# Optimization experiments

Measured on AMD Instinct MI355X. Metric: run time of the kernel, lower is better.

## Reference

```python
import jax, jax.numpy as jnp
import numpy as np

N_NODES = 100000
N_EDGES = 1600000
IN_F = 32
HID_F = 128  # unused by the torch module's GCN (only conv1), kept for fidelity
OUT_F = 64


def setup_inputs() -> dict:
    key = jax.random.key(0)
    ks = jax.random.split(key, 8)
    x = jax.random.normal(ks[0], (N_NODES, IN_F), dtype=jnp.float32)
    edge_index = jax.random.randint(ks[1], (2, N_EDGES), 0, N_NODES, dtype=jnp.int64)
    s = 1.0 / np.sqrt(IN_F)
    # SAGEConv params: lin_l acts on mean-aggregated neighbors (with bias), lin_r on root
    W_l = jax.random.uniform(ks[2], (IN_F, OUT_F), minval=-s, maxval=s, dtype=jnp.float32)
    W_r = jax.random.uniform(ks[3], (IN_F, OUT_F), minval=-s, maxval=s, dtype=jnp.float32)
    b_l = jnp.zeros((OUT_F,), dtype=jnp.float32)
    # MLPPredictor: lin1 (2*OUT_F -> OUT_F), lin2 (OUT_F -> 1)
    s1 = 1.0 / np.sqrt(2 * OUT_F)
    W1 = jax.random.uniform(ks[4], (2 * OUT_F, OUT_F), minval=-s1, maxval=s1, dtype=jnp.float32)
    b1 = jnp.zeros((OUT_F,), dtype=jnp.float32)
    s2 = 1.0 / np.sqrt(OUT_F)
    W2 = jax.random.uniform(ks[5], (OUT_F, 1), minval=-s2, maxval=s2, dtype=jnp.float32)
    b2 = jnp.zeros((1,), dtype=jnp.float32)
    return {"x": x, "edge_index": edge_index, "W_l": W_l, "W_r": W_r, "b_l": b_l,
            "W1": W1, "b1": b1, "W2": W2, "b2": b2}


def reference(x, edge_index, W_l, W_r, b_l, W1, b1, W2, b2):
    src = edge_index[0]  # sender / message source
    dst = edge_index[1]  # receiver / aggregation target
    n = x.shape[0]
    # SAGEConv with mean aggregation: out_i = lin_l(mean_{j->i} x_j) + lin_r(x_i)
    agg = jax.ops.segment_sum(x[src], dst, num_segments=n)  # [N, IN_F]
    cnt = jax.ops.segment_sum(jnp.ones((src.shape[0],), x.dtype), dst, num_segments=n)
    mean_agg = agg / jnp.maximum(cnt, 1.0)[:, None]
    h = jnp.tanh(mean_agg @ W_l + b_l + x @ W_r)  # [N, OUT_F]
    # MLPPredictor: per-edge concat(sender, receiver) -> lin1 -> tanh -> lin2 -> tanh
    he = jnp.concatenate([h[src], h[dst]], axis=-1)  # [E, 2*OUT_F]
    he = jnp.tanh(he @ W1 + b1)
    he = jnp.tanh(he @ W2 + b2)  # [E, 1]
    return jax.nn.sigmoid(he)
```

## Files before the change

kernel.cpp:

```cpp
#include <hip/hip_runtime.h>
#include <hip/hip_bf16.h>

#define NN 100000
#define NE 1600000
#define INF 32
#define OUTF 64

typedef __hip_bfloat16 bf16;
typedef unsigned long long u64;
typedef __attribute__((ext_vector_type(8))) short short8v;
typedef __attribute__((ext_vector_type(4))) float float4v;
typedef __attribute__((ext_vector_type(2))) float floatx2;

__device__ __forceinline__ float load_f(const void* p, long long i, int f32) {
  return f32 ? ((const float*)p)[i] : __bfloat162float(((const bf16*)p)[i]);
}
__device__ __forceinline__ int load_idx(const void* p, long long i, int i64) {
  return i64 ? (int)((const long long*)p)[i] : ((const int*)p)[i];
}
__device__ __forceinline__ float fast_tanh(float x) {
  float e = __expf(2.0f * x);
  return 1.0f - 2.0f * __builtin_amdgcn_rcpf(e + 1.0f);
}
__device__ __forceinline__ bf16 f2b(float f) { return __float2bfloat16(f); }
__device__ __forceinline__ short bf_bits(float f) {
  bf16 h = __float2bfloat16(f);
  return *reinterpret_cast<short*>(&h);
}
__device__ __forceinline__ unsigned enc_fx(float v) {
  v = fminf(fmaxf(v, -7.99f), 7.99f);
  return (unsigned)rintf((v + 8.0f) * 64.0f);
}
__device__ __forceinline__ unsigned char f2fp8(float f) {
  unsigned p = __builtin_amdgcn_cvt_pk_fp8_f32(f, f, 0, false);
  return (unsigned char)(p & 0xFF);
}

__global__ void k_detect(const void* __restrict__ x, const void* __restrict__ ei,
                         int* __restrict__ flags)
{
  int t = threadIdx.x;
  const unsigned* xu = (const unsigned*)x;
  int hits = 0;
  #pragma unroll
  for (int i = 0; i < 16; ++i) {
    unsigned w = xu[t * 16 + i];
    unsigned mid = (w >> 7) & 0xFF;
    hits += (mid >= 0x70 && mid <= 0x86) ? 1 : 0;
  }
  #pragma unroll
  for (int off = 32; off > 0; off >>= 1) hits += __shfl_xor(hits, off, 64);
  const int* e32 = (const int*)ei;
  unsigned long long m = __ballot(e32[2 * t + 1] == 0);
  if (t == 0) {
    flags[0] = (hits < 512) ? 1 : 0;
    flags[1] = (m == ~0ULL) ? 1 : 0;
  }
}

__global__ __launch_bounds__(256)
void k_prep(const void* __restrict__ x, u64* __restrict__ penc,
            const int* __restrict__ flags)
{
  int xf32 = flags[0];
  int i = blockIdx.x * 256 + threadIdx.x;
  float v0, v1, v2, v3;
  if (xf32) {
    float4 v = ((const float4*)x)[i];
    v0 = v.x; v1 = v.y; v2 = v.z; v3 = v.w;
  } else {
    uint2 w = ((const uint2*)x)[i];
    v0 = __uint_as_float(w.x << 16);
    v1 = __uint_as_float(w.x & 0xffff0000u);
    v2 = __uint_as_float(w.y << 16);
    v3 = __uint_as_float(w.y & 0xffff0000u);
  }
  penc[i] = (u64)enc_fx(v0) | ((u64)enc_fx(v1) << 16)
          | ((u64)enc_fx(v2) << 32) | ((u64)enc_fx(v3) << 48);
}

__global__ __launch_bounds__(256)
void k_agg(const u64* __restrict__ penc, const void* __restrict__ ei,
           u64* __restrict__ pa, int* __restrict__ icnt,
           const int* __restrict__ flags)
{
  int ei64 = flags[1];
  long long gid = (long long)blockIdx.x * 256 + threadIdx.x;
  int e = (int)(gid >> 3);
  int lane = threadIdx.x & 63;
  int q = lane & 7;
  int iv = 0;
  if (q < 2) iv = load_idx(ei, (q ? (long long)NE : 0) + e, ei64);
  int base = lane & ~7;
  int src = __shfl(iv, base, 64);
  int dst = __shfl(iv, base | 1, 64);
  u64 pk = penc[(long long)src * 8 + q];
  atomicAdd(&pa[(long long)dst * 8 + q], pk);
  if (q == 0) atomicAdd(&icnt[dst], 1);
}

__global__ __launch_bounds__(256)
void k_node_uv(const void* __restrict__ x, const u64* __restrict__ pa,
               const int* __restrict__ icnt,
               const void* __restrict__ Wl, const void* __restrict__ Wr,
               const void* __restrict__ bl,
               const void* __restrict__ W1, const void* __restrict__ b1,
               unsigned char* __restrict__ U8, unsigned char* __restrict__ V8,
               const int* __restrict__ flags)
{
  __shared__ bf16 sh[4][16][64];
  __shared__ __align__(16) unsigned char sU[4][16][64];
  __shared__ __align__(16) unsigned char sV[4][16][64];
  int xf32 = flags[0];
  int lane = threadIdx.x & 63, wv = threadIdx.x >> 6;
  int r = lane & 15, g = lane >> 4;

  short8v Bh[2][4];
  #pragma unroll
  for (int kb = 0; kb < 2; ++kb) {
    const void* W = kb ? Wr : Wl;
    #pragma unroll
    for (int nb = 0; nb < 4; ++nb) {
      short8v v;
      #pragma unroll
      for (int e = 0; e < 8; ++e)
        v[e] = bf_bits(load_f(W, (long long)(8 * g + e) * 64 + nb * 16 + r, xf32));
      Bh[kb][nb] = v;
    }
  }
  short8v Bf[4][4];
  #pragma unroll
  for (int kb = 0; kb < 4; ++kb)
    #pragma unroll
    for (int nb = 0; nb < 4; ++nb) {
      short8v v;
      #pragma unroll
      for (int e = 0; e < 8; ++e)
        v[e] = bf_bits(load_f(W1, (long long)(kb * 32 + 8 * g + e) * 64 + nb * 16 + r, xf32));
      Bf[kb][nb] = v;
    }
  float blv[4], b1v[4];
  #pragma unroll
  for (int nb = 0; nb < 4; ++nb) {
    blv[nb] = load_f(bl, nb * 16 + r, xf32);
    b1v[nb] = load_f(b1, nb * 16 + r, xf32);
  }

  const int NT2 = NN / 16;
  int nw = gridDim.x * 4;
  for (int t = blockIdx.x * 4 + wv; t < NT2; t += nw) {
    int n0 = t * 16;
    int node = n0 + r;
    int cnt = icnt[node];
    float s = (cnt > 0) ? __builtin_amdgcn_rcpf(64.0f * cnt) : 0.0f;
    float bias = (cnt > 0) ? 8.0f : 0.0f;
    u64 p0 = pa[(long long)node * 8 + 2 * g];
    u64 p1 = pa[(long long)node * 8 + 2 * g + 1];
    short8v A0, A1;
    #pragma unroll
    for (int j = 0; j < 4; ++j) {
      A0[j]     = bf_bits((float)((p0 >> (16 * j)) & 0xffff) * s - bias);
      A0[4 + j] = bf_bits((float)((p1 >> (16 * j)) & 0xffff) * s - bias);
    }
    if (xf32) {
      const float* xp = (const float*)x + (long long)node * 32 + 8 * g;
      #pragma unroll
      for (int e = 0; e < 8; ++e) A1[e] = bf_bits(xp[e]);
    } else {
      A1 = *(const short8v*)((const bf16*)x + (long long)node * 32 + 8 * g);
    }

    #pragma unroll
    for (int nb = 0; nb < 4; ++nb) {
      float4v acc = (float4v){blv[nb], blv[nb], blv[nb], blv[nb]};
      acc = __builtin_amdgcn_mfma_f32_16x16x32_bf16(A0, Bh[0][nb], acc, 0, 0, 0);
      acc = __builtin_amdgcn_mfma_f32_16x16x32_bf16(A1, Bh[1][nb], acc, 0, 0, 0);
      #pragma unroll
      for (int j = 0; j < 4; ++j)
        sh[wv][4 * g + j][nb * 16 + r] = f2b(fast_tanh(acc[j]));
    }
    asm volatile("s_waitcnt lgkmcnt(0)" ::: "memory");
    __builtin_amdgcn_sched_barrier(0);
    short8v Ah0 = *(const short8v*)&sh[wv][r][8 * g];
    short8v Ah1 = *(const short8v*)&sh[wv][r][32 + 8 * g];

    #pragma unroll
    for (int nb = 0; nb < 4; ++nb) {
      float4v au = (float4v){b1v[nb], b1v[nb], b1v[nb], b1v[nb]};
      au = __builtin_amdgcn_mfma_f32_16x16x32_bf16(Ah0, Bf[0][nb], au, 0, 0, 0);
      au = __builtin_amdgcn_mfma_f32_16x16x32_bf16(Ah1, Bf[1][nb], au, 0, 0, 0);
      float4v av = (float4v){0.0f, 0.0f, 0.0f, 0.0f};
      av = __builtin_amdgcn_mfma_f32_16x16x32_bf16(Ah0, Bf[2][nb], av, 0, 0, 0);
      av = __builtin_amdgcn_mfma_f32_16x16x32_bf16(Ah1, Bf[3][nb], av, 0, 0, 0);
      #pragma unroll
      for (int j = 0; j < 4; ++j) {
        sU[wv][4 * g + j][nb * 16 + r] = f2fp8(au[j]);
        sV[wv][4 * g + j][nb * 16 + r] = f2fp8(av[j]);
      }
    }
    asm volatile("s_waitcnt lgkmcnt(0)" ::: "memory");
    __builtin_amdgcn_sched_barrier(0);

    uint4 stu = *(const uint4*)&sU[wv][r][g * 16];
    uint4 stv = *(const uint4*)&sV[wv][r][g * 16];
    *(uint4*)(U8 + (long long)(n0 + r) * 64 + g * 16) = stu;
    *(uint4*)(V8 + (long long)(n0 + r) * 64 + g * 16) = stv;
    asm volatile("s_waitcnt lgkmcnt(0)" ::: "memory");
    __builtin_amdgcn_sched_barrier(0);
  }
}

struct UV8 { uint4 u, v; };

__device__ __forceinline__ int ld_idx16(const void* ei, long long t, int NT,
                                        int lane, int ei64)
{
  long long tt = (t < NT) ? t : (NT - 1);
  long long e0 = tt * 16;
  int iv = 0;
  if (lane < 32) {
    long long off = (lane < 16) ? (e0 + lane) : ((long long)NE + e0 + (lane - 16));
    iv = ei64 ? (int)((const long long*)ei)[off] : ((const int*)ei)[off];
  }
  return iv;
}
__device__ __forceinline__ UV8 ld_uv8(const unsigned char* U8, const unsigned char* V8,
                                      int iv, int e4, int j)
{
  int sB = __shfl(iv, e4, 64);
  int dB = __shfl(iv, 16 + e4, 64);
  UV8 f;
  f.u = *(const uint4*)(U8 + (long long)sB * 64 + j * 16);
  f.v = *(const uint4*)(V8 + (long long)dB * 64 + j * 16);
  return f;
}

__global__ __launch_bounds__(256)
void k_edge2(const unsigned char* __restrict__ U8, const unsigned char* __restrict__ V8,
             const void* __restrict__ ei,
             const void* __restrict__ W2, const void* __restrict__ b2,
             void* __restrict__ outv, const int* __restrict__ flags)
{
  int xf32 = flags[0], ei64 = flags[1];
  int lane = threadIdx.x & 63, wv = threadIdx.x >> 6;
  int e4 = lane >> 2, j = lane & 3;
  float w2v[16];
  #pragma unroll
  for (int i = 0; i < 16; ++i) w2v[i] = load_f(W2, 16 * j + i, xf32);
  float b2v = load_f(b2, 0, xf32);

  const int NT = NE / 16;
  int nw = gridDim.x * 4;
  long long w0 = blockIdx.x * 4 + wv;

  int i0 = ld_idx16(ei, w0, NT, lane, ei64);
  int i1 = ld_idx16(ei, w0 + nw, NT, lane, ei64);
  int i2 = ld_idx16(ei, w0 + 2 * (long long)nw, NT, lane, ei64);
  UV8 uv0 = ld_uv8(U8, V8, i0, e4, j);
  UV8 uv1 = ld_uv8(U8, V8, i1, e4, j);

  for (long long t = w0; t < NT; t += nw) {
    int i3 = ld_idx16(ei, t + 3 * (long long)nw, NT, lane, ei64);
    UV8 uv2 = ld_uv8(U8, V8, i2, e4, j);

    unsigned ua[4] = {uv0.u.x, uv0.u.y, uv0.u.z, uv0.u.w};
    unsigned va[4] = {uv0.v.x, uv0.v.y, uv0.v.z, uv0.v.w};
    float z = 0.0f;
    #pragma unroll
    for (int d = 0; d < 4; ++d) {
      floatx2 ul = __builtin_amdgcn_cvt_pk_f32_fp8(ua[d], false);
      floatx2 uh = __builtin_amdgcn_cvt_pk_f32_fp8(ua[d], true);
      floatx2 vl = __builtin_amdgcn_cvt_pk_f32_fp8(va[d], false);
      floatx2 vh = __builtin_amdgcn_cvt_pk_f32_fp8(va[d], true);
      z += fast_tanh(ul.x + vl.x) * w2v[4 * d + 0];
      z += fast_tanh(ul.y + vl.y) * w2v[4 * d + 1];
      z += fast_tanh(uh.x + vh.x) * w2v[4 * d + 2];
      z += fast_tanh(uh.y + vh.y) * w2v[4 * d + 3];
    }
    z += __shfl_xor(z, 1, 64);
    z += __shfl_xor(z, 2, 64);
    if (j == 0) {
      float y = fast_tanh(z + b2v);
      float res = __builtin_amdgcn_rcpf(1.0f + __expf(-y));
      long long eo = t * 16 + e4;
      if (xf32) ((float*)outv)[eo] = res;
      else      ((bf16*)outv)[eo] = f2b(res);
    }
    i2 = i3;
    uv0 = uv1;
    uv1 = uv2;
  }
}

extern "C" void kernel_launch(void* const* d_in, const int* in_sizes, int n_in,
                              void* d_out, int out_size, void* d_ws, size_t ws_size,
                              hipStream_t stream)
{
  const void* x  = d_in[0];
  const void* ei = d_in[1];
  const void* Wl = d_in[2];
  const void* Wr = d_in[3];
  const void* bl = d_in[4];
  const void* W1 = d_in[5];
  const void* b1 = d_in[6];
  const void* W2 = d_in[7];
  const void* b2 = d_in[8];

  char* ws = (char*)d_ws;
  u64*  pa    = (u64*)ws;
  int*  icnt  = (int*)(ws + 6400000);
  int*  flags = (int*)(ws + 6800000);
  u64*  penc  = (u64*)(ws + 6800128);
  unsigned char* U8 = (unsigned char*)(ws + 13200128);
  unsigned char* V8 = (unsigned char*)(ws + 19600128);

  k_detect<<<1, 64, 0, stream>>>(x, ei, flags);
  hipMemsetAsync(pa, 0, 6800000, stream);

  k_prep<<<(NN * 8) / 256, 256, 0, stream>>>(x, penc, flags);
  k_agg<<<(NE * 8) / 256, 256, 0, stream>>>(penc, ei, pa, icnt, flags);
  k_node_uv<<<512, 256, 0, stream>>>(x, pa, icnt, Wl, Wr, bl, W1, b1, U8, V8, flags);
  k_edge2<<<2048, 256, 0, stream>>>(U8, V8, ei, W2, b2, d_out, flags);
}
```

Baseline: 319.1 us.

## Replace atomic fixed-point scatter aggregation with CSR sort and segmented mean

The per-edge 64-bit atomic scatter of fixed-point encoded features is replaced by a counting sort of edges by destination (histogram, three-pass scan, atomic scatter of source ids), followed by a gather-based segmented mean that writes bf16 means directly. The node kernel now reads the precomputed bf16 mean instead of decoding fixed-point sums, and its grid grows. The aim is to remove the heavy contention of 8 atomics per edge on the aggregation buffer, at the cost of several extra launches and an atomic scatter pass. Workspace buffers are reused between stages (U8/V8 alias xb and sorted).

```diff
diff --git a/kernel.cpp b/kernel.cpp
--- a/kernel.cpp
+++ b/kernel.cpp
@@ -23,13 +23,12 @@
   return 1.0f - 2.0f * __builtin_amdgcn_rcpf(e + 1.0f);
 }
 __device__ __forceinline__ bf16 f2b(float f) { return __float2bfloat16(f); }
-__device__ __forceinline__ short bf_bits(float f) {
+__device__ __forceinline__ unsigned short bf_bits(float f) {
   bf16 h = __float2bfloat16(f);
-  return *reinterpret_cast<short*>(&h);
-}
-__device__ __forceinline__ unsigned enc_fx(float v) {
-  v = fminf(fmaxf(v, -7.99f), 7.99f);
-  return (unsigned)rintf((v + 8.0f) * 64.0f);
+  return *reinterpret_cast<unsigned short*>(&h);
+}
+__device__ __forceinline__ float s2f(unsigned short s) {
+  return __uint_as_float(((unsigned)s) << 16);
 }
 __device__ __forceinline__ unsigned char f2fp8(float f) {
   unsigned p = __builtin_amdgcn_cvt_pk_fp8_f32(f, f, 0, false);
@@ -59,49 +58,122 @@
 }
 
 __global__ __launch_bounds__(256)
-void k_prep(const void* __restrict__ x, u64* __restrict__ penc,
-            const int* __restrict__ flags)
+void k_xb(const void* __restrict__ x, u64* __restrict__ xb,
+          const int* __restrict__ flags)
 {
   int xf32 = flags[0];
   int i = blockIdx.x * 256 + threadIdx.x;
-  float v0, v1, v2, v3;
   if (xf32) {
     float4 v = ((const float4*)x)[i];
-    v0 = v.x; v1 = v.y; v2 = v.z; v3 = v.w;
+    xb[i] = (u64)bf_bits(v.x) | ((u64)bf_bits(v.y) << 16)
+          | ((u64)bf_bits(v.z) << 32) | ((u64)bf_bits(v.w) << 48);
   } else {
-    uint2 w = ((const uint2*)x)[i];
-    v0 = __uint_as_float(w.x << 16);
-    v1 = __uint_as_float(w.x & 0xffff0000u);
-    v2 = __uint_as_float(w.y << 16);
-    v3 = __uint_as_float(w.y & 0xffff0000u);
-  }
-  penc[i] = (u64)enc_fx(v0) | ((u64)enc_fx(v1) << 16)
-          | ((u64)enc_fx(v2) << 32) | ((u64)enc_fx(v3) << 48);
-}
-
-__global__ __launch_bounds__(256)
-void k_agg(const u64* __restrict__ penc, const void* __restrict__ ei,
-           u64* __restrict__ pa, int* __restrict__ icnt,
-           const int* __restrict__ flags)
+    xb[i] = ((const u64*)x)[i];
+  }
+}
+
+__global__ __launch_bounds__(256)
+void k_hist(const void* __restrict__ ei, int* __restrict__ cnt,
+            const int* __restrict__ flags)
 {
   int ei64 = flags[1];
-  long long gid = (long long)blockIdx.x * 256 + threadIdx.x;
-  int e = (int)(gid >> 3);
-  int lane = threadIdx.x & 63;
-  int q = lane & 7;
-  int iv = 0;
-  if (q < 2) iv = load_idx(ei, (q ? (long long)NE : 0) + e, ei64);
-  int base = lane & ~7;
-  int src = __shfl(iv, base, 64);
-  int dst = __shfl(iv, base | 1, 64);
-  u64 pk = penc[(long long)src * 8 + q];
-  atomicAdd(&pa[(long long)dst * 8 + q], pk);
-  if (q == 0) atomicAdd(&icnt[dst], 1);
-}
-
-__global__ __launch_bounds__(256)
-void k_node_uv(const void* __restrict__ x, const u64* __restrict__ pa,
-               const int* __restrict__ icnt,
+  int e = blockIdx.x * 256 + threadIdx.x;
+  int dst = load_idx(ei, (long long)NE + e, ei64);
+  atomicAdd(&cnt[dst], 1);
+}
+
+__global__ __launch_bounds__(256)
+void k_scan1(const int* __restrict__ cnt, int* __restrict__ off,
+             int* __restrict__ sums)
+{
+  __shared__ int s[256];
+  int t = threadIdx.x;
+  int i = blockIdx.x * 256 + t;
+  int v = (i < NN) ? cnt[i] : 0;
+  s[t] = v;
+  __syncthreads();
+  #pragma unroll
+  for (int d = 1; d < 256; d <<= 1) {
+    int y = (t >= d) ? s[t - d] : 0;
+    __syncthreads();
+    s[t] += y;
+    __syncthreads();
+  }
+  if (i < NN) off[i] = s[t] - v;
+  if (t == 255) sums[blockIdx.x] = s[255];
+}
+
+__global__ __launch_bounds__(512)
+void k_scan2(int* __restrict__ sums)
+{
+  __shared__ int s[512];
+  int t = threadIdx.x;
+  int v = (t < 391) ? sums[t] : 0;
+  s[t] = v;
+  __syncthreads();
+  #pragma unroll
+  for (int d = 1; d < 512; d <<= 1) {
+    int y = (t >= d) ? s[t - d] : 0;
+    __syncthreads();
+    s[t] += y;
+    __syncthreads();
+  }
+  if (t < 391) sums[t] = s[t] - v;
+}
+
+__global__ __launch_bounds__(256)
+void k_scan3(int* __restrict__ off, int* __restrict__ off2,
+             const int* __restrict__ sums)
+{
+  int i = blockIdx.x * 256 + threadIdx.x;
+  if (i < NN) {
+    int o = off[i] + sums[blockIdx.x];
+    off[i] = o;
+    off2[i] = o;
+  }
+}
+
+__global__ __launch_bounds__(256)
+void k_scatter(const void* __restrict__ ei, int* __restrict__ off2,
+               int* __restrict__ sorted, const int* __restrict__ flags)
+{
+  int ei64 = flags[1];
+  int e = blockIdx.x * 256 + threadIdx.x;
+  int src = load_idx(ei, e, ei64);
+  int dst = load_idx(ei, (long long)NE + e, ei64);
+  int pos = atomicAdd(&off2[dst], 1);
+  sorted[pos] = src;
+}
+
+__global__ __launch_bounds__(256)
+void k_segmean(const u64* __restrict__ xb, const int* __restrict__ sorted,
+               const int* __restrict__ off, const int* __restrict__ cnt,
+               u64* __restrict__ meanb)
+{
+  int lane = threadIdx.x & 63, wv = threadIdx.x >> 6;
+  int grp = lane >> 3, q = lane & 7;
+  int dst = (blockIdx.x * 4 + wv) * 8 + grp;
+  int begin = off[dst];
+  int n = cnt[dst];
+  float a0 = 0.f, a1 = 0.f, a2 = 0.f, a3 = 0.f;
+  int src = (n > 0) ? sorted[begin] : 0;
+  for (int k = 0; k < n; ++k) {
+    int srcN = (k + 1 < n) ? sorted[begin + k + 1] : 0;
+    u64 w = xb[(long long)src * 8 + q];
+    a0 += s2f((unsigned short)(w & 0xffff));
+    a1 += s2f((unsigned short)((w >> 16) & 0xffff));
+    a2 += s2f((unsigned short)((w >> 32) & 0xffff));
+    a3 += s2f((unsigned short)((w >> 48) & 0xffff));
+    src = srcN;
+  }
+  float sc = __builtin_amdgcn_rcpf(fmaxf((float)n, 1.0f));
+  meanb[(long long)dst * 8 + q] =
+      (u64)bf_bits(a0 * sc) | ((u64)bf_bits(a1 * sc) << 16)
+    | ((u64)bf_bits(a2 * sc) << 32) | ((u64)bf_bits(a3 * sc) << 48);
+}
+
+__global__ __launch_bounds__(256)
+void k_node_uv(const void* __restrict__ x, const u64* __restrict__ meanb,
                const void* __restrict__ Wl, const void* __restrict__ Wr,
                const void* __restrict__ bl,
                const void* __restrict__ W1, const void* __restrict__ b1,
@@ -124,7 +196,7 @@
       short8v v;
       #pragma unroll
       for (int e = 0; e < 8; ++e)
-        v[e] = bf_bits(load_f(W, (long long)(8 * g + e) * 64 + nb * 16 + r, xf32));
+        v[e] = (short)bf_bits(load_f(W, (long long)(8 * g + e) * 64 + nb * 16 + r, xf32));
       Bh[kb][nb] = v;
     }
   }
@@ -136,7 +208,7 @@
       short8v v;
       #pragma unroll
       for (int e = 0; e < 8; ++e)
-        v[e] = bf_bits(load_f(W1, (long long)(kb * 32 + 8 * g + e) * 64 + nb * 16 + r, xf32));
+        v[e] = (short)bf_bits(load_f(W1, (long long)(kb * 32 + 8 * g + e) * 64 + nb * 16 + r, xf32));
       Bf[kb][nb] = v;
     }
   float blv[4], b1v[4];
@@ -151,21 +223,12 @@
   for (int t = blockIdx.x * 4 + wv; t < NT2; t += nw) {
     int n0 = t * 16;
     int node = n0 + r;
-    int cnt = icnt[node];
-    float s = (cnt > 0) ? __builtin_amdgcn_rcpf(64.0f * cnt) : 0.0f;
-    float bias = (cnt > 0) ? 8.0f : 0.0f;
-    u64 p0 = pa[(long long)node * 8 + 2 * g];
-    u64 p1 = pa[(long long)node * 8 + 2 * g + 1];
-    short8v A0, A1;
-    #pragma unroll
-    for (int j = 0; j < 4; ++j) {
-      A0[j]     = bf_bits((float)((p0 >> (16 * j)) & 0xffff) * s - bias);
-      A0[4 + j] = bf_bits((float)((p1 >> (16 * j)) & 0xffff) * s - bias);
-    }
+    short8v A0 = *(const short8v*)((const char*)meanb + (long long)node * 64 + g * 16);
+    short8v A1;
     if (xf32) {
       const float* xp = (const float*)x + (long long)node * 32 + 8 * g;
       #pragma unroll
-      for (int e = 0; e < 8; ++e) A1[e] = bf_bits(xp[e]);
+      for (int e = 0; e < 8; ++e) A1[e] = (short)bf_bits(xp[e]);
     } else {
       A1 = *(const short8v*)((const bf16*)x + (long long)node * 32 + 8 * g);
     }
@@ -307,18 +370,27 @@
   const void* b2 = d_in[8];
 
   char* ws = (char*)d_ws;
-  u64*  pa    = (u64*)ws;
-  int*  icnt  = (int*)(ws + 6400000);
-  int*  flags = (int*)(ws + 6800000);
-  u64*  penc  = (u64*)(ws + 6800128);
-  unsigned char* U8 = (unsigned char*)(ws + 13200128);
-  unsigned char* V8 = (unsigned char*)(ws + 19600128);
+  int* flags  = (int*)(ws);
+  int* cnt    = (int*)(ws + 1024);
+  int* off    = (int*)(ws + 401408);
+  int* off2   = (int*)(ws + 801792);
+  int* sums   = (int*)(ws + 1202176);
+  int* sorted = (int*)(ws + 1208320);
+  u64* xb     = (u64*)(ws + 7608320);
+  u64* meanb  = (u64*)(ws + 14008320);
+  unsigned char* U8 = (unsigned char*)(ws + 7608320);
+  unsigned char* V8 = (unsigned char*)(ws + 1208320);
 
   k_detect<<<1, 64, 0, stream>>>(x, ei, flags);
-  hipMemsetAsync(pa, 0, 6800000, stream);
-
-  k_prep<<<(NN * 8) / 256, 256, 0, stream>>>(x, penc, flags);
-  k_agg<<<(NE * 8) / 256, 256, 0, stream>>>(penc, ei, pa, icnt, flags);
-  k_node_uv<<<512, 256, 0, stream>>>(x, pa, icnt, Wl, Wr, bl, W1, b1, U8, V8, flags);
+  hipMemsetAsync(cnt, 0, 400000, stream);
+
+  k_xb<<<3125, 256, 0, stream>>>(x, xb, flags);
+  k_hist<<<6250, 256, 0, stream>>>(ei, cnt, flags);
+  k_scan1<<<391, 256, 0, stream>>>(cnt, off, sums);
+  k_scan2<<<1, 512, 0, stream>>>(sums);
+  k_scan3<<<391, 256, 0, stream>>>(off, off2, sums);
+  k_scatter<<<6250, 256, 0, stream>>>(ei, off2, sorted, flags);
+  k_segmean<<<3125, 256, 0, stream>>>(xb, sorted, off, cnt, meanb);
+  k_node_uv<<<1563, 256, 0, stream>>>(x, meanb, Wl, Wr, bl, W1, b1, U8, V8, flags);
   k_edge2<<<2048, 256, 0, stream>>>(U8, V8, ei, W2, b2, d_out, flags);
 }
```

Result: slower. 461.7 us (+44.7%).
